# Kernel tuning notes

Measured on AMD Instinct MI355X. Metric: run time of the kernel, lower is better.

The kernel has to match this reference:

```python
import jax, jax.numpy as jnp
import numpy as np
from jax.scipy.special import betainc, ndtri, ndtr

DF = 4.0        # fixed_df
ALPHA = 0.94    # ewma_alpha
EPS = 1e-5      # scale_eps
UCLIP = 1e-6    # cdf clamp


def _ewma_loc_scale(x_hist):
    # x_hist: [B, T, D]
    loc = jnp.mean(x_hist, axis=1, keepdims=True)            # [B,1,D]
    c2 = jnp.square(x_hist - loc)                            # [B,T,D]
    c2_t = jnp.swapaxes(c2, 0, 1)                            # [T,B,D] for scan over time

    def step(var, c):
        var = ALPHA * var + (1.0 - ALPHA) * c
        return var, var

    _, tail = jax.lax.scan(step, c2_t[0], c2_t[1:])
    ewma = jnp.concatenate([c2_t[:1], tail], axis=0)         # [T,B,D]
    ewma = jnp.swapaxes(ewma, 0, 1)                          # [B,T,D]
    scale_hist = jnp.maximum(jnp.sqrt(ewma * (DF - 2.0) / DF), EPS)
    return loc, scale_hist


def _student_t_cdf(x, loc, scale):
    # Student-t CDF via regularized incomplete beta: df fixed scalar constant
    t = (x - loc) / scale
    w = DF / (DF + t * t)
    p = 0.5 * betainc(DF / 2.0, 0.5, w)
    u = jnp.where(t <= 0.0, p, 1.0 - p)
    return jnp.clip(u, UCLIP, 1.0 - UCLIP)


def _student_t_ppf_df4(u):
    # Exact closed form for df=4 (Shaw): a = 4u(1-u),
    # q = sign(u-1/2) * 2*sqrt(cos(arccos(sqrt(a))/3)/sqrt(a) - 1)
    a = jnp.clip(4.0 * u * (1.0 - u), UCLIP, 1.0)
    sa = jnp.sqrt(a)
    inner = jnp.cos(jnp.arccos(sa) / 3.0) / sa - 1.0
    q = 2.0 * jnp.sqrt(jnp.maximum(inner, 0.0))
    return jnp.sign(u - 0.5) * q


def setup_inputs() -> dict:
    key = jax.random.key(0)
    k1, k2 = jax.random.split(key)
    B, T, P, D = 128, 2048, 64, 128
    x_hist = jax.random.normal(k1, (B, T, D), dtype=jnp.float32)
    z_future = jax.random.normal(k2, (B, P, D), dtype=jnp.float32)
    return {"x_hist": x_hist, "z_future": z_future}


def reference(x_hist, z_future):
    # _fit_student_t: loc + EWMA variance -> per-step scale
    loc, scale_hist = _ewma_loc_scale(x_hist)                # [B,1,D], [B,T,D]
    scale_future = scale_hist[:, -1:, :]                     # [B,1,D]
    # _to_gaussian(x_hist): t CDF -> standard normal ICDF
    x_hist_norm = ndtri(_student_t_cdf(x_hist, loc, scale_hist))  # [B,T,D]
    # _from_gaussian(z_future): normal CDF -> t PPF (df=4 closed form)
    u = jnp.clip(ndtr(z_future), UCLIP, 1.0 - UCLIP)
    forecasts = _student_t_ppf_df4(u) * scale_future + loc   # [B,P,D]
    # concat along time for a single output tensor [B, T+P, D]
    return jnp.concatenate([x_hist_norm, forecasts], axis=1)
```

## Files before the change

### kernel.cpp

```cpp
#include <hip/hip_runtime.h>
#include <math.h>

namespace {
constexpr int B = 128;
constexpr int T = 2048;
constexpr int D = 128;
constexpr int P = 64;
constexpr int TOUT = T + P;
constexpr int NC = 32;
constexpr int L = T / NC;
constexpr float ALPHA = 0.94f;
constexpr float OMA = (float)(1.0 - 0.94);
constexpr float UCLIP = 1e-6f;
constexpr float SQRT2 = 1.41421356237309515f;
constexpr float INV_SQRT2 = 0.70710678118654752f;
constexpr float RMAX = 0.999998f;
}

__device__ __forceinline__ float fast_erfinv(float x) {
    float w = -__logf((1.0f - x) * (1.0f + x));
    float p;
    if (w < 5.0f) {
        w -= 2.5f;
        p = 2.81022636e-08f;
        p = fmaf(p, w, 3.43273939e-07f);
        p = fmaf(p, w, -3.5233877e-06f);
        p = fmaf(p, w, -4.39150654e-06f);
        p = fmaf(p, w, 0.00021858087f);
        p = fmaf(p, w, -0.00125372503f);
        p = fmaf(p, w, -0.00417768164f);
        p = fmaf(p, w, 0.246640727f);
        p = fmaf(p, w, 1.50140941f);
    } else {
        w = sqrtf(w) - 3.0f;
        p = -0.000200214257f;
        p = fmaf(p, w, 0.000100950558f);
        p = fmaf(p, w, 0.00134934322f);
        p = fmaf(p, w, -0.00367342844f);
        p = fmaf(p, w, 0.00573950773f);
        p = fmaf(p, w, -0.0076224613f);
        p = fmaf(p, w, 0.00943887047f);
        p = fmaf(p, w, 1.00167406f);
        p = fmaf(p, w, 2.83297682f);
    }
    return p * x;
}

__device__ __forceinline__ float t_to_z(float xv, float mu, float e1, float e2) {
    float ew = fmaxf(fmaf(mu, mu, fmaf(-2.0f * mu, e1, e2)), 0.0f);
    float v = fmaxf(0.5f * ew, 1e-10f);
    float inv_scale = rsqrtf(v);
    float tt = (xv - mu) * inv_scale;
    float t2 = tt * tt;
    float ig = rsqrtf(4.0f + t2);
    float r = tt * (6.0f + t2) * (ig * ig * ig);
    r = fminf(fmaxf(r, -RMAX), RMAX);
    return SQRT2 * fast_erfinv(r);
}

__global__ __launch_bounds__(128) void kA(const float* __restrict__ x,
                                          float* __restrict__ Spart,
                                          float* __restrict__ l1e,
                                          float* __restrict__ l2e) {
    const int c = blockIdx.x;
    const int b = blockIdx.y;
    const int d = threadIdx.x;

    const float* xp = x + ((size_t)b * T + (size_t)c * L) * D + d;

    float x0 = xp[0];
    float sum = x0;
    float l1, l2;
    if (c == 0) { l1 = x0;        l2 = x0 * x0; }
    else        { l1 = OMA * x0;  l2 = OMA * (x0 * x0); }

    for (int k = 1; k < L; ++k) {
        float xv = xp[(size_t)k * D];
        sum += xv;
        l1 = ALPHA * l1 + OMA * xv;
        l2 = ALPHA * l2 + OMA * (xv * xv);
    }

    const size_t o = ((size_t)b * NC + c) * D + d;
    Spart[o] = sum;
    l1e[o]   = l1;
    l2e[o]   = l2;
}

__global__ __launch_bounds__(256) void kB(const float* Spart,
                                          const float* l1e,
                                          const float* l2e,
                                          float* carry1,
                                          float* carry2,
                                          float* __restrict__ loc,
                                          float* __restrict__ scf) {
    const int tid = blockIdx.x * blockDim.x + threadIdx.x;
    if (tid >= B * D) return;
    const int b = tid / D;
    const int d = tid % D;

    const float alphaL = (float)pow((double)ALPHA, (double)L);

    float sum = 0.0f, e1 = 0.0f, e2 = 0.0f;
    for (int c = 0; c < NC; ++c) {
        const size_t o = ((size_t)b * NC + c) * D + d;
        float sp = Spart[o];
        float t1 = l1e[o];
        float t2 = l2e[o];
        carry1[o] = e1;
        carry2[o] = e2;
        sum += sp;
        e1 = t1 + alphaL * e1;
        e2 = t2 + alphaL * e2;
    }

    const float mu = sum * (1.0f / (float)T);
    loc[tid] = mu;
    float ew = fmaxf(fmaf(mu, mu, fmaf(-2.0f * mu, e1, e2)), 0.0f);
    scf[tid] = fmaxf(sqrtf(0.5f * ew), 1e-5f);
}

__global__ __launch_bounds__(128) void kC(const float* __restrict__ x,
                                          const float* __restrict__ carry1,
                                          const float* __restrict__ carry2,
                                          const float* __restrict__ loc,
                                          float* __restrict__ out) {
    const int c = blockIdx.x;
    const int b = blockIdx.y;
    const int d = threadIdx.x;

    const size_t co = ((size_t)b * NC + c) * D + d;
    const float cr1 = carry1[co];
    const float cr2 = carry2[co];
    const float mu  = loc[b * D + d];

    const float* xp = x   + ((size_t)b * T    + (size_t)c * L) * D + d;
    float*       op = out + ((size_t)b * TOUT + (size_t)c * L) * D + d;

    float xv = xp[0];
    float l1, l2;
    if (c == 0) { l1 = xv;       l2 = xv * xv; }
    else        { l1 = OMA * xv; l2 = OMA * (xv * xv); }
    float f = ALPHA;
    op[0] = t_to_z(xv, mu, l1 + f * cr1, l2 + f * cr2);

    for (int k = 1; k < L; ++k) {
        xv = xp[(size_t)k * D];
        l1 = ALPHA * l1 + OMA * xv;
        l2 = ALPHA * l2 + OMA * (xv * xv);
        f *= ALPHA;
        op[(size_t)k * D] = t_to_z(xv, mu, l1 + f * cr1, l2 + f * cr2);
    }
}

__global__ __launch_bounds__(256) void kD(const float* __restrict__ zf,
                                          const float* __restrict__ loc,
                                          const float* __restrict__ scf,
                                          float* __restrict__ out) {
    const int idx = blockIdx.x * blockDim.x + threadIdx.x;
    if (idx >= B * P * D) return;
    const int d  = idx % D;
    const int bp = idx / D;
    const int p  = bp % P;
    const int b  = bp / P;

    float zv = zf[idx];
    float u = 0.5f * erfcf(-zv * INV_SQRT2);
    u = fminf(fmaxf(u, UCLIP), 1.0f - UCLIP);

    float a = 4.0f * u * (1.0f - u);
    a = fminf(fmaxf(a, UCLIP), 1.0f);
    float sa = sqrtf(a);
    float inner = cosf(acosf(sa) * (1.0f / 3.0f)) / sa - 1.0f;
    float q = 2.0f * sqrtf(fmaxf(inner, 0.0f));

    float sgn = (u > 0.5f) ? 1.0f : ((u < 0.5f) ? -1.0f : 0.0f);
    float val = sgn * q * scf[b * D + d] + loc[b * D + d];

    out[((size_t)b * TOUT + T + p) * D + d] = val;
}

extern "C" void kernel_launch(void* const* d_in, const int* in_sizes, int n_in,
                              void* d_out, int out_size, void* d_ws, size_t ws_size,
                              hipStream_t stream) {
    const float* x  = (const float*)d_in[0];
    const float* zf = (const float*)d_in[1];
    float* out = (float*)d_out;

    float* ws = (float*)d_ws;
    const size_t NCH = (size_t)B * NC * D;
    float* Spart  = ws;
    float* l1e    = Spart + NCH;
    float* l2e    = l1e + NCH;
    float* loc    = l2e + NCH;
    float* scf    = loc + (size_t)B * D;
    float* carry1 = Spart;
    float* carry2 = l1e;

    kA<<<dim3(NC, B), 128, 0, stream>>>(x, Spart, l1e, l2e);
    kB<<<(B * D + 255) / 256, 256, 0, stream>>>(Spart, l1e, l2e, carry1, carry2, loc, scf);
    kC<<<dim3(NC, B), 128, 0, stream>>>(x, carry1, carry2, loc, out);
    kD<<<(B * P * D + 255) / 256, 256, 0, stream>>>(zf, loc, scf, out);
}
```

Measured before the change: 96.18 us.

## Fold mean into single EWMA recurrence, skip scale divide, and double chunk count

kC now runs one recurrence on x*(x-2mu) instead of separate first and second moment recurrences. kB folds the two carries into one combined carry, so kC loads less and does less arithmetic per element. The t-statistic is computed from unscaled deviation and variance, which removes an rsqrt per element. NC goes from 32 to 64 to double the block count for kA and kC, at the cost of a longer serial carry loop in kB and a larger workspace.

Result: slower. 101.6 us (+5.6%).

```diff
diff --git a/kernel.cpp b/kernel.cpp
--- a/kernel.cpp
+++ b/kernel.cpp
@@ -7,7 +7,7 @@
 constexpr int D = 128;
 constexpr int P = 64;
 constexpr int TOUT = T + P;
-constexpr int NC = 32;
+constexpr int NC = 64;
 constexpr int L = T / NC;
 constexpr float ALPHA = 0.94f;
 constexpr float OMA = (float)(1.0 - 0.94);
@@ -18,7 +18,7 @@
 }
 
 __device__ __forceinline__ float fast_erfinv(float x) {
-    float w = -__logf((1.0f - x) * (1.0f + x));
+    float w = -__logf(fmaf(-x, x, 1.0f));
     float p;
     if (w < 5.0f) {
         w -= 2.5f;
@@ -46,14 +46,13 @@
     return p * x;
 }
 
-__device__ __forceinline__ float t_to_z(float xv, float mu, float e1, float e2) {
-    float ew = fmaxf(fmaf(mu, mu, fmaf(-2.0f * mu, e1, e2)), 0.0f);
-    float v = fmaxf(0.5f * ew, 1e-10f);
-    float inv_scale = rsqrtf(v);
-    float tt = (xv - mu) * inv_scale;
-    float t2 = tt * tt;
-    float ig = rsqrtf(4.0f + t2);
-    float r = tt * (6.0f + t2) * (ig * ig * ig);
+__device__ __forceinline__ float t_to_z(float y, float v) {
+    float y2 = y * y;
+    float a6 = fmaf(v, 6.0f, y2);
+    float a4 = fmaf(v, 4.0f, y2);
+    float m  = rsqrtf(a4);
+    float m3 = m * m * m;
+    float r  = y * a6 * m3;
     r = fminf(fmaxf(r, -RMAX), RMAX);
     return SQRT2 * fast_erfinv(r);
 }
@@ -118,38 +117,46 @@
     loc[tid] = mu;
     float ew = fmaxf(fmaf(mu, mu, fmaf(-2.0f * mu, e1, e2)), 0.0f);
     scf[tid] = fmaxf(sqrtf(0.5f * ew), 1e-5f);
+
+    for (int c = 0; c < NC; ++c) {
+        const size_t o = ((size_t)b * NC + c) * D + d;
+        float c1 = carry1[o];
+        float c2 = carry2[o];
+        carry1[o] = fmaf(-2.0f * mu, c1, c2);
+    }
 }
 
 __global__ __launch_bounds__(128) void kC(const float* __restrict__ x,
-                                          const float* __restrict__ carry1,
-                                          const float* __restrict__ carry2,
-                                          const float* __restrict__ loc,
+                                          const float* __restrict__ crw_buf,
+                                          const float* __restrict__ locg,
                                           float* __restrict__ out) {
     const int c = blockIdx.x;
     const int b = blockIdx.y;
     const int d = threadIdx.x;
 
     const size_t co = ((size_t)b * NC + c) * D + d;
-    const float cr1 = carry1[co];
-    const float cr2 = carry2[co];
-    const float mu  = loc[b * D + d];
+    const float crw   = crw_buf[co];
+    const float mu    = locg[b * D + d];
+    const float twomu = 2.0f * mu;
+    const float mu2h  = 0.5f * mu * mu;
 
     const float* xp = x   + ((size_t)b * T    + (size_t)c * L) * D + d;
     float*       op = out + ((size_t)b * TOUT + (size_t)c * L) * D + d;
 
     float xv = xp[0];
-    float l1, l2;
-    if (c == 0) { l1 = xv;       l2 = xv * xv; }
-    else        { l1 = OMA * xv; l2 = OMA * (xv * xv); }
-    float f = ALPHA;
-    op[0] = t_to_z(xv, mu, l1 + f * cr1, l2 + f * cr2);
+    float g  = xv * (xv - twomu);
+    float lw = (c == 0) ? g : OMA * g;
+    float f  = ALPHA;
+    float vv = fmaxf(fmaf(0.5f, fmaf(f, crw, lw), mu2h), 1e-10f);
+    op[0] = t_to_z(xv - mu, vv);
 
     for (int k = 1; k < L; ++k) {
         xv = xp[(size_t)k * D];
-        l1 = ALPHA * l1 + OMA * xv;
-        l2 = ALPHA * l2 + OMA * (xv * xv);
+        g  = xv * (xv - twomu);
+        lw = fmaf(ALPHA, lw, OMA * g);
         f *= ALPHA;
-        op[(size_t)k * D] = t_to_z(xv, mu, l1 + f * cr1, l2 + f * cr2);
+        vv = fmaxf(fmaf(0.5f, fmaf(f, crw, lw), mu2h), 1e-10f);
+        op[(size_t)k * D] = t_to_z(xv - mu, vv);
     }
 }
 
@@ -199,6 +206,6 @@
 
     kA<<<dim3(NC, B), 128, 0, stream>>>(x, Spart, l1e, l2e);
     kB<<<(B * D + 255) / 256, 256, 0, stream>>>(Spart, l1e, l2e, carry1, carry2, loc, scf);
-    kC<<<dim3(NC, B), 128, 0, stream>>>(x, carry1, carry2, loc, out);
+    kC<<<dim3(NC, B), 128, 0, stream>>>(x, carry1, loc, out);
     kD<<<(B * P * D + 255) / 256, 256, 0, stream>>>(zf, loc, scf, out);
 }
```
